# Optimization experiments

Hardware: AMD Instinct MI355X
Metric: run time of the kernel (lower is better)

Reference implementation:

```python
import jax, jax.numpy as jnp
import numpy as np
import math

B, S, D, H = 2, 2048, 1024, 16
HD = D // H  # head dim = 64


def setup_inputs() -> dict:
    key = jax.random.key(0)
    k1, k2, k3, k4, k5 = jax.random.split(key, 5)
    query = jax.random.normal(k1, (B, S, D), dtype=jnp.float32)
    # tail padding: sequence lengths 1536 and 1792 -> positions >= length are padded (True)
    lengths = jnp.array([1536, 1792], dtype=jnp.int32)
    padding_mask = jnp.arange(S, dtype=jnp.int32)[None, :] >= lengths[:, None]  # [B,S] bool
    qkv_w = jax.random.normal(k2, (3 * D, D), dtype=jnp.float32) * 0.02
    qkv_b = jax.random.uniform(k3, (3 * D,), dtype=jnp.float32, minval=-0.03, maxval=0.03)
    out_w = jax.random.normal(k4, (D, D), dtype=jnp.float32) * 0.02
    out_b = jax.random.uniform(k5, (D,), dtype=jnp.float32, minval=-0.03, maxval=0.03)
    return {"query": query, "padding_mask": padding_mask,
            "qkv_w": qkv_w, "qkv_b": qkv_b, "out_w": out_w, "out_b": out_b}


def reference(query, padding_mask, qkv_w, qkv_b, out_w, out_b):
    # self-attention path (qkv_same=True): fused qkv projection then split
    qkv = query @ qkv_w.T + qkv_b                      # [B,S,3D]
    q, k, v = jnp.split(qkv, 3, axis=-1)               # each [B,S,D]

    def split_heads(x):
        return x.reshape(B, S, H, HD).transpose(0, 2, 1, 3)  # [B,H,S,HD]

    q, k, v = split_heads(q), split_heads(k), split_heads(v)

    # scores scaled by sqrt(head_dim)
    w = jnp.einsum('bhqd,bhkd->bhqk', q, k) / math.sqrt(HD)  # [B,H,S,S]

    # causal (future) mask: strict upper triangle masked
    future = jnp.triu(jnp.ones((S, S), dtype=bool), 1)
    w = jnp.where(future[None, None, :, :], -jnp.inf, w)
    # key padding mask
    w = jnp.where(padding_mask[:, None, None, :], -jnp.inf, w)

    a = jax.nn.softmax(w, axis=-1)
    # rows of fully-padded sequences are zeroed (dropout is identity in eval)
    all_masked = jnp.all(padding_mask, axis=-1)        # [B]
    a = jnp.where(all_masked[:, None, None, None], 0.0, a)

    x = jnp.einsum('bhqk,bhkd->bhqd', a, v)            # [B,H,S,HD]
    x = x.transpose(0, 2, 1, 3).reshape(B, S, D)       # merge heads
    return x @ out_w.T + out_b
```

## Files before the change

kernel.cpp:

```cpp
#include <hip/hip_runtime.h>
#include <hip/hip_bf16.h>
#include <stdint.h>

#define S_  2048
#define B_  2
#define H_  16
#define D_  1024
#define HD_ 64

typedef short short8 __attribute__((ext_vector_type(8)));
typedef float f32x4  __attribute__((ext_vector_type(4)));

__device__ __forceinline__ unsigned short bf16_rne(float f) {
  unsigned int u = __float_as_uint(f);
  u += 0x7fffu + ((u >> 16) & 1u);
  return (unsigned short)(u >> 16);
}

__device__ __forceinline__ f32x4 mfma_bf16(short8 a, short8 b, f32x4 c) {
  return __builtin_amdgcn_mfma_f32_16x16x32_bf16(a, b, c, 0, 0, 0);
}

__global__ void cvt3_kernel(const float* __restrict__ a, unsigned short* __restrict__ oa, int na8,
                            const float* __restrict__ b, unsigned short* __restrict__ ob, int nb8,
                            const float* __restrict__ c, unsigned short* __restrict__ oc, int nc8) {
  int i = blockIdx.x * blockDim.x + threadIdx.x;
  const float* in; unsigned short* out; int idx;
  if (i < na8) { in = a; out = oa; idx = i; }
  else if (i < na8 + nb8) { in = b; out = ob; idx = i - na8; }
  else if (i < na8 + nb8 + nc8) { in = c; out = oc; idx = i - na8 - nb8; }
  else return;
  const float4* p = (const float4*)in + (size_t)idx * 2;
  float4 x = p[0], y = p[1];
  union { unsigned short u[8]; short8 v; } r;
  r.u[0] = bf16_rne(x.x); r.u[1] = bf16_rne(x.y);
  r.u[2] = bf16_rne(x.z); r.u[3] = bf16_rne(x.w);
  r.u[4] = bf16_rne(y.x); r.u[5] = bf16_rne(y.y);
  r.u[6] = bf16_rne(y.z); r.u[7] = bf16_rne(y.w);
  *((short8*)out + idx) = r.v;
}

__global__ void lengths_kernel(const void* __restrict__ mask, int* __restrict__ lens) {
  __shared__ int mn[B_];
  __shared__ int anyb;
  int t = threadIdx.x;
  if (t < B_) mn[t] = S_;
  if (t == 0) anyb = 0;
  __syncthreads();
  const unsigned char* mb = (const unsigned char*)mask;
  for (int i = t; i < B_ * S_; i += 256) {
    if (mb[i]) { anyb = 1; atomicMin(&mn[i >> 11], i & (S_ - 1)); }
  }
  __syncthreads();
  if (!anyb) {
    const int* mi = (const int*)mask;
    for (int i = t; i < B_ * S_; i += 256) {
      if (mi[i]) atomicMin(&mn[i >> 11], i & (S_ - 1));
    }
    __syncthreads();
  }
  if (t < B_) lens[t] = mn[t];
}

__global__ __launch_bounds__(256) void gemm_bt_kernel(
    const unsigned short* __restrict__ A,
    const unsigned short* __restrict__ W,
    int K, int N, int mode,
    const float* __restrict__ bias,
    unsigned short* __restrict__ qb,
    unsigned short* __restrict__ kb,
    unsigned short* __restrict__ vb,
    float* __restrict__ outf) {
  __shared__ unsigned short As[128 * 32];
  __shared__ unsigned short Bs[128 * 32];
  const int tile_m = blockIdx.y * 128;
  const int tile_n = blockIdx.x * 128;
  const int t = threadIdx.x;
  const int lane = t & 63;
  const int w = t >> 6;
  const int wr = w >> 1, wc = w & 1;
  const int l15 = lane & 15, lk = lane >> 4;

  f32x4 acc[4][4];
#pragma unroll
  for (int i = 0; i < 4; i++)
#pragma unroll
    for (int j = 0; j < 4; j++) { f32x4 z = {0.f, 0.f, 0.f, 0.f}; acc[i][j] = z; }

  for (int k0 = 0; k0 < K; k0 += 32) {
#pragma unroll
    for (int c = 0; c < 2; ++c) {
      int e = (c * 256 + t) * 8;
      int row = e >> 5, col = e & 31;
      __builtin_amdgcn_global_load_lds(
          (__attribute__((address_space(1))) void*)(A + (size_t)(tile_m + row) * K + k0 + col),
          (__attribute__((address_space(3))) void*)(&As[e]), 16, 0, 0);
      __builtin_amdgcn_global_load_lds(
          (__attribute__((address_space(1))) void*)(W + (size_t)(tile_n + row) * K + k0 + col),
          (__attribute__((address_space(3))) void*)(&Bs[e]), 16, 0, 0);
    }
    asm volatile("s_waitcnt vmcnt(0)" ::: "memory");
    __syncthreads();

    short8 af[4], bfr[4];
#pragma unroll
    for (int i = 0; i < 4; i++)
      af[i] = *(const short8*)&As[(wr * 64 + i * 16 + l15) * 32 + lk * 8];
#pragma unroll
    for (int j = 0; j < 4; j++)
      bfr[j] = *(const short8*)&Bs[(wc * 64 + j * 16 + l15) * 32 + lk * 8];
#pragma unroll
    for (int i = 0; i < 4; i++)
#pragma unroll
      for (int j = 0; j < 4; j++)
        acc[i][j] = mfma_bf16(af[i], bfr[j], acc[i][j]);
    __syncthreads();
  }

#pragma unroll
  for (int i = 0; i < 4; i++) {
#pragma unroll
    for (int j = 0; j < 4; j++) {
      int gn = tile_n + wc * 64 + j * 16 + l15;
      float bv = bias[gn];
#pragma unroll
      for (int r = 0; r < 4; r++) {
        int gm = tile_m + wr * 64 + i * 16 + lk * 4 + r;
        float v = acc[i][j][r] + bv;
        if (mode == 0) {
          int bb = gm >> 11, s = gm & (S_ - 1);
          int which = gn >> 10, dd = gn & (D_ - 1);
          int h = dd >> 6, d = dd & 63;
          size_t dst = ((size_t)((bb * H_ + h) * S_ + s)) * HD_ + d;
          unsigned short* dstp = (which == 0) ? qb : (which == 1) ? kb : vb;
          dstp[dst] = bf16_rne(which == 0 ? v * 0.125f : v);
        } else {
          outf[(size_t)gm * N + gn] = v;
        }
      }
    }
  }
}

__global__ __launch_bounds__(512) void attn_kernel(
    const unsigned short* __restrict__ qbuf,
    const unsigned short* __restrict__ kbuf,
    const unsigned short* __restrict__ vbuf,
    const int* __restrict__ lens,
    unsigned short* __restrict__ attn_out) {
  __shared__ __align__(16) char smem[51200];

  const int bid = blockIdx.x;
  const int virt = ((bid & 7) << 7) | (bid >> 3);
  const int bh = virt >> 5;
  const int qt = virt & 31;
  const int b = bh >> 4;
  const int len = lens[b];
  const int t = threadIdx.x;
  const int lane = t & 63, w = t >> 6;
  const int g = w >> 2, wg = w & 3;
  const int l15 = lane & 15, lk = lane >> 4;
  const int qbase = qt * 64 + wg * 16;

  unsigned short* Ks = (unsigned short*)(smem + g * 8192);
  unsigned int*   Vt = (unsigned int*)(smem + 16384 + g * 9216);
  unsigned short* Ps = (unsigned short*)(smem + 34816 + (w << 11));

  const unsigned short* qbh = qbuf + (size_t)bh * S_ * HD_;
  const unsigned short* kbh = kbuf + (size_t)bh * S_ * HD_;
  const unsigned short* vbh = vbuf + (size_t)bh * S_ * HD_;

  const int qrow = qbase + l15;
  const short8 qf0 = *(const short8*)&qbh[(size_t)qrow * HD_ + lk * 8];
  const short8 qf1 = *(const short8*)&qbh[(size_t)qrow * HD_ + 32 + lk * 8];

  f32x4 o[4];
#pragma unroll
  for (int n = 0; n < 4; n++) { f32x4 z = {0.f, 0.f, 0.f, 0.f}; o[n] = z; }
  float rsum[4] = {0.f, 0.f, 0.f, 0.f};

  const int ke = (len - 1) >> 6;
  const int kt_end = qt < ke ? qt : ke;
  const int NI = (kt_end >> 1) + 1;

  const int tg = t & 255;
  const int vr2 = tg & 31, vcg = tg >> 5;
  const int kr0 = tg >> 3, kc0 = tg & 7;

  short8 pk0 = {}, pk1 = {}, pv0 = {}, pv1 = {};

#define LDG(KT)                                                               \
  {                                                                           \
    int ks0_ = (KT) * 64;                                                     \
    pk0 = *(const short8*)&kbh[(size_t)(ks0_ + kr0) * HD_ + kc0 * 8];         \
    pk1 = *(const short8*)&kbh[(size_t)(ks0_ + kr0 + 32) * HD_ + kc0 * 8];    \
    const unsigned short* vp = vbh + (size_t)(ks0_ + 2 * vr2) * HD_ + vcg * 8;\
    pv0 = *(const short8*)vp;                                                 \
    pv1 = *(const short8*)(vp + HD_);                                         \
  }

  int my_kt = g;
  bool act = (my_kt <= kt_end);
  if (act) LDG(my_kt);

  for (int i = 0; i < NI; ++i) {
    __syncthreads();
    if (act) {
      *(short8*)&Ks[kr0 * 64 + ((kc0 ^ (kr0 & 7)) << 3)] = pk0;
      int r1 = kr0 + 32;
      *(short8*)&Ks[r1 * 64 + ((kc0 ^ (r1 & 7)) << 3)] = pk1;
#pragma unroll
      for (int j = 0; j < 8; j++) {
        int d = vcg * 8 + j;
        unsigned int pk = (unsigned int)(unsigned short)pv0[j] |
                          ((unsigned int)(unsigned short)pv1[j] << 16);
        Vt[d * 36 + ((((vr2 >> 1) ^ (d & 15)) << 1) | (vr2 & 1))] = pk;
      }
    }
    __syncthreads();
    const int nxt = my_kt + 2;
    const bool nact = (nxt <= kt_end);
    if (nact) LDG(nxt);

    if (act) {
      const int ks0 = my_kt * 64;
      f32x4 sc[4];
#pragma unroll
      for (int j = 0; j < 4; j++) {
        int krow = j * 16 + l15;
        const short8 kf0 =
            *(const short8*)&Ks[krow * 64 + ((lk ^ (krow & 7)) << 3)];
        const short8 kf1 =
            *(const short8*)&Ks[krow * 64 + (((4 | lk) ^ (krow & 7)) << 3)];
        f32x4 a = {0.f, 0.f, 0.f, 0.f};
        a = mfma_bf16(qf0, kf0, a);
        a = mfma_bf16(qf1, kf1, a);
        sc[j] = a;
      }
      if ((my_kt == qt) || (ks0 + 63 >= len)) {
#pragma unroll
        for (int j = 0; j < 4; j++)
#pragma unroll
          for (int r = 0; r < 4; r++) {
            int q = qbase + lk * 4 + r;
            int kk = ks0 + j * 16 + l15;
            if (kk > q || kk >= len) sc[j][r] = -1e30f;
          }
      }
#pragma unroll
      for (int j = 0; j < 4; j++)
#pragma unroll
        for (int r = 0; r < 4; r++) {
          float p = __expf(sc[j][r]);
          rsum[r] += p;
          int qr = lk * 4 + r;
          Ps[qr * 64 + ((j * 16 + l15) ^ ((qr & 7) << 3))] = bf16_rne(p);
        }
#pragma unroll
      for (int ks2 = 0; ks2 < 2; ++ks2) {
        const short8 pf = *(const short8*)
            &Ps[l15 * 64 + ((ks2 * 32 + lk * 8) ^ ((l15 & 7) << 3))];
        const int g0 = ks2 * 8 + lk * 2;
#pragma unroll
        for (int n = 0; n < 4; n++) {
          int d = n * 16 + l15;
          uint2 w0 = *(const uint2*)&Vt[d * 36 + ((g0 ^ l15) << 1)];
          uint2 w1 = *(const uint2*)&Vt[d * 36 + (((g0 + 1) ^ l15) << 1)];
          union { unsigned int u[4]; short8 s; } vv;
          vv.u[0] = w0.x; vv.u[1] = w0.y; vv.u[2] = w1.x; vv.u[3] = w1.y;
          o[n] = mfma_bf16(pf, vv.s, o[n]);
        }
      }
    }
    my_kt = nxt; act = nact;
  }
#undef LDG

#pragma unroll
  for (int r = 0; r < 4; r++) {
#pragma unroll
    for (int d = 1; d < 16; d <<= 1) rsum[r] += __shfl_xor(rsum[r], d, 64);
  }

  float* mo = (float*)smem;
  float* ml = (float*)(smem + 16896);
  __syncthreads();
  if (g == 1) {
#pragma unroll
    for (int r = 0; r < 4; r++) {
      int row = wg * 16 + lk * 4 + r;
#pragma unroll
      for (int n = 0; n < 4; n++) mo[row * 66 + n * 16 + l15] = o[n][r];
      if (l15 == 0) ml[row] = rsum[r];
    }
  }
  __syncthreads();
  if (g == 0) {
#pragma unroll
    for (int r = 0; r < 4; r++) {
      int row = wg * 16 + lk * 4 + r;
      float lt = rsum[r] + ml[row];
      float inv = (lt > 0.f) ? (1.0f / lt) : 0.f;
      int s = qt * 64 + row;
#pragma unroll
      for (int n = 0; n < 4; n++) {
        float ot = o[n][r] + mo[row * 66 + n * 16 + l15];
        attn_out[((size_t)(b * S_ + s)) * D_ + (bh & 15) * HD_ + n * 16 + l15] =
            bf16_rne(ot * inv);
      }
    }
  }
}

extern "C" void kernel_launch(void* const* d_in, const int* in_sizes, int n_in,
                              void* d_out, int out_size, void* d_ws, size_t ws_size,
                              hipStream_t stream) {
  const float* query = (const float*)d_in[0];
  const void*  mask  = d_in[1];
  const float* qkv_w = (const float*)d_in[2];
  const float* qkv_b = (const float*)d_in[3];
  const float* out_w = (const float*)d_in[4];
  const float* out_b = (const float*)d_in[5];
  float* out = (float*)d_out;

  char* ws = (char*)d_ws;
  unsigned short* qx     = (unsigned short*)(ws);
  unsigned short* wqkv   = (unsigned short*)(ws + (8u  << 20));
  unsigned short* wout   = (unsigned short*)(ws + (14u << 20));
  unsigned short* qbuf   = (unsigned short*)(ws + (16u << 20));
  unsigned short* kbuf   = (unsigned short*)(ws + (24u << 20));
  unsigned short* vbuf   = (unsigned short*)(ws + (32u << 20));
  unsigned short* attn_o = qx;
  int* lens              = (int*)(ws + (40u << 20));

  lengths_kernel<<<1, 256, 0, stream>>>(mask, lens);
  const int na8 = B_ * S_ * D_ / 8, nb8 = 3 * D_ * D_ / 8, nc8 = D_ * D_ / 8;
  cvt3_kernel<<<(na8 + nb8 + nc8) / 256, 256, 0, stream>>>(
      query, qx, na8, qkv_w, wqkv, nb8, out_w, wout, nc8);

  dim3 g1(3 * D_ / 128, B_ * S_ / 128);
  gemm_bt_kernel<<<g1, 256, 0, stream>>>(qx, wqkv, D_, 3 * D_, 0, qkv_b,
                                         qbuf, kbuf, vbuf, nullptr);

  attn_kernel<<<1024, 512, 0, stream>>>(qbuf, kbuf, vbuf, lens, attn_o);

  dim3 g2(D_ / 128, B_ * S_ / 128);
  gemm_bt_kernel<<<g2, 256, 0, stream>>>(attn_o, wout, D_, D_, 1, out_b,
                                         nullptr, nullptr, nullptr, out);
}
```

Measured before the change: 152.1 us.

## Replace QKV projection GEMM with 256x256 double-buffered direct-to-LDS pipelined kernel

Adds a new QKV projection kernel that uses 256x256 tiles with 8 waves, global_load_lds async copies into XOR-swizzled double-buffered LDS, and interleaves the staging of the next K-chunk with the MFMA phases, raising MFMA priority with setprio. The grid is also remapped across XCDs. The goal is to hide global memory latency and raise data reuse compared with the old 128x128 single-buffered GEMM. The old GEMM is cut down to the output-projection path only. This adds complexity and uses 128KB of LDS, and with 192 workgroups the GPU may be underfilled.

```diff
diff --git a/kernel.cpp b/kernel.cpp
--- a/kernel.cpp
+++ b/kernel.cpp
@@ -62,14 +62,140 @@
   if (t < B_) lens[t] = mn[t];
 }
 
+__global__ __launch_bounds__(512, 2) void gemm8p_kernel(
+    const unsigned short* __restrict__ A,
+    const unsigned short* __restrict__ W,
+    int K, int NBX,
+    const float* __restrict__ bias,
+    unsigned short* __restrict__ qb,
+    unsigned short* __restrict__ kb,
+    unsigned short* __restrict__ vb) {
+  __shared__ __align__(16) unsigned short lds[65536];
+
+  const int nwg = gridDim.x;
+  const int cpx = nwg >> 3;
+  const int bid = blockIdx.x;
+  const int virt = (bid & 7) * cpx + (bid >> 3);
+  const int bx = virt % NBX, by = virt / NBX;
+  const int tile_m = by * 256, tile_n = bx * 256;
+  const int t = threadIdx.x;
+  const int lane = t & 63, w = t >> 6;
+  const int wm = w >> 2, wn = w & 3;
+  const int l15 = lane & 15, lk = lane >> 4;
+  const int NT = K >> 6;
+
+  f32x4 acc[8][4];
+#pragma unroll
+  for (int i = 0; i < 8; i++)
+#pragma unroll
+    for (int j = 0; j < 4; j++) { f32x4 z = {0.f, 0.f, 0.f, 0.f}; acc[i][j] = z; }
+
+  const int L0 = t, L1 = 512 + t;
+  const int r0 = L0 >> 3, c0 = (L0 & 7) ^ (r0 & 7);
+  const int r1 = L1 >> 3, c1 = (L1 & 7) ^ (r1 & 7);
+
+#define STAGE_HALF(SRC, GROW0, DSTE, KC)                                      \
+  {                                                                           \
+    __builtin_amdgcn_global_load_lds(                                         \
+        (const __attribute__((address_space(1))) void*)(                      \
+            (SRC) + (size_t)((GROW0) + r0) * K + (KC) + c0 * 8),              \
+        (__attribute__((address_space(3))) void*)(&lds[(DSTE) + L0 * 8]),     \
+        16, 0, 0);                                                            \
+    __builtin_amdgcn_global_load_lds(                                         \
+        (const __attribute__((address_space(1))) void*)(                      \
+            (SRC) + (size_t)((GROW0) + r1) * K + (KC) + c1 * 8),              \
+        (__attribute__((address_space(3))) void*)(&lds[(DSTE) + L1 * 8]),     \
+        16, 0, 0);                                                            \
+  }
+
+  STAGE_HALF(A, tile_m,        0,    0);
+  STAGE_HALF(W, tile_n,        32768, 0);
+  STAGE_HALF(A, tile_m + 128,  8192, 0);
+  STAGE_HALF(W, tile_n + 128,  32768 + 8192, 0);
+  asm volatile("s_waitcnt vmcnt(4)" ::: "memory");
+  __builtin_amdgcn_s_barrier();
+
+  for (int tc = 0; tc < NT; ++tc) {
+    const int cb = (tc & 1) * 16384;
+    const int ob = ((tc & 1) ^ 1) * 16384;
+    int tn = tc + 1; if (tn >= NT) tn = NT - 1;
+    const int k0n = tn << 6;
+
+#pragma unroll
+    for (int p = 0; p < 4; ++p) {
+      const int mh = (p & 1);
+      const int nh = (p >> 1);
+      short8 af[4][2], bfr[2][2];
+#pragma unroll
+      for (int fi = 0; fi < 4; ++fi) {
+        const int rl = fi * 32 + wm * 16 + l15;
+#pragma unroll
+        for (int ks = 0; ks < 2; ++ks) {
+          const int sw = (ks * 4 + lk) ^ (rl & 7);
+          af[fi][ks] = *(const short8*)&lds[cb + mh * 8192 + rl * 64 + sw * 8];
+        }
+      }
+#pragma unroll
+      for (int fj = 0; fj < 2; ++fj) {
+        const int cl = wn * 32 + fj * 16 + l15;
+#pragma unroll
+        for (int ks = 0; ks < 2; ++ks) {
+          const int sw = (ks * 4 + lk) ^ (cl & 7);
+          bfr[fj][ks] =
+              *(const short8*)&lds[32768 + cb + nh * 8192 + cl * 64 + sw * 8];
+        }
+      }
+      if (p == 0)      STAGE_HALF(A, tile_m,       ob,                k0n)
+      else if (p == 1) STAGE_HALF(W, tile_n,       32768 + ob,        k0n)
+      else if (p == 2) STAGE_HALF(A, tile_m + 128, ob + 8192,         k0n)
+      else             STAGE_HALF(W, tile_n + 128, 32768 + ob + 8192, k0n);
+      if (p != 2) asm volatile("s_waitcnt vmcnt(4)" ::: "memory");
+      else        asm volatile("" ::: "memory");
+      __builtin_amdgcn_s_barrier();
+      asm volatile("s_waitcnt lgkmcnt(0)" ::: "memory");
+      __builtin_amdgcn_s_setprio(1);
+#pragma unroll
+      for (int fi = 0; fi < 4; ++fi)
+#pragma unroll
+        for (int fj = 0; fj < 2; ++fj)
+#pragma unroll
+          for (int ks = 0; ks < 2; ++ks)
+            acc[mh * 4 + fi][nh * 2 + fj] =
+                mfma_bf16(af[fi][ks], bfr[fj][ks], acc[mh * 4 + fi][nh * 2 + fj]);
+      __builtin_amdgcn_s_setprio(0);
+      __builtin_amdgcn_s_barrier();
+    }
+  }
+  asm volatile("s_waitcnt vmcnt(0)" ::: "memory");
+#undef STAGE_HALF
+
+#pragma unroll
+  for (int j = 0; j < 4; ++j) {
+    const int gn = tile_n + (j >> 1) * 128 + wn * 32 + (j & 1) * 16 + l15;
+    const float bv = bias[gn];
+    const int which = gn >> 10, dd = gn & (D_ - 1);
+    const int h = dd >> 6, d = dd & 63;
+    unsigned short* dstp = (which == 0) ? qb : (which == 1) ? kb : vb;
+    const float mul = (which == 0) ? 0.125f : 1.0f;
+#pragma unroll
+    for (int i = 0; i < 8; ++i) {
+      const int gmb = tile_m + (i >> 2) * 128 + (i & 3) * 32 + wm * 16 + lk * 4;
+#pragma unroll
+      for (int r = 0; r < 4; ++r) {
+        const int gm = gmb + r;
+        const int bb = gm >> 11, s = gm & (S_ - 1);
+        dstp[((size_t)((bb * H_ + h) * S_ + s)) * HD_ + d] =
+            bf16_rne((acc[i][j][r] + bv) * mul);
+      }
+    }
+  }
+}
+
 __global__ __launch_bounds__(256) void gemm_bt_kernel(
     const unsigned short* __restrict__ A,
     const unsigned short* __restrict__ W,
-    int K, int N, int mode,
+    int K, int N,
     const float* __restrict__ bias,
-    unsigned short* __restrict__ qb,
-    unsigned short* __restrict__ kb,
-    unsigned short* __restrict__ vb,
     float* __restrict__ outf) {
   __shared__ unsigned short As[128 * 32];
   __shared__ unsigned short Bs[128 * 32];
@@ -126,17 +252,7 @@
 #pragma unroll
       for (int r = 0; r < 4; r++) {
         int gm = tile_m + wr * 64 + i * 16 + lk * 4 + r;
-        float v = acc[i][j][r] + bv;
-        if (mode == 0) {
-          int bb = gm >> 11, s = gm & (S_ - 1);
-          int which = gn >> 10, dd = gn & (D_ - 1);
-          int h = dd >> 6, d = dd & 63;
-          size_t dst = ((size_t)((bb * H_ + h) * S_ + s)) * HD_ + d;
-          unsigned short* dstp = (which == 0) ? qb : (which == 1) ? kb : vb;
-          dstp[dst] = bf16_rne(which == 0 ? v * 0.125f : v);
-        } else {
-          outf[(size_t)gm * N + gn] = v;
-        }
+        outf[(size_t)gm * N + gn] = acc[i][j][r] + bv;
       }
     }
   }
@@ -338,13 +454,11 @@
   cvt3_kernel<<<(na8 + nb8 + nc8) / 256, 256, 0, stream>>>(
       query, qx, na8, qkv_w, wqkv, nb8, out_w, wout, nc8);
 
-  dim3 g1(3 * D_ / 128, B_ * S_ / 128);
-  gemm_bt_kernel<<<g1, 256, 0, stream>>>(qx, wqkv, D_, 3 * D_, 0, qkv_b,
-                                         qbuf, kbuf, vbuf, nullptr);
+  gemm8p_kernel<<<192, 512, 0, stream>>>(qx, wqkv, D_, 3 * D_ / 256, qkv_b,
+                                         qbuf, kbuf, vbuf);
 
   attn_kernel<<<1024, 512, 0, stream>>>(qbuf, kbuf, vbuf, lens, attn_o);
 
   dim3 g2(D_ / 128, B_ * S_ / 128);
-  gemm_bt_kernel<<<g2, 256, 0, stream>>>(attn_o, wout, D_, D_, 1, out_b,
-                                         nullptr, nullptr, nullptr, out);
-}
+  gemm_bt_kernel<<<g2, 256, 0, stream>>>(attn_o, wout, D_, D_, out_b, out);
+}
```

After: 147.0 us. 3.3% less time.
